# Optimization experiments

Hardware: AMD Instinct MI355X
Metric: run time of the kernel (lower is better)

The kernel has to match this reference:

```python
import jax, jax.numpy as jnp
import numpy as np

I = 2048   # input_size
H = 2048   # hidden_size
O = 1024   # output_size (decode steps AND out-linear width)
LEAK = 0.01  # nn.LeakyReLU default negative_slope


def setup_inputs() -> dict:
    key = jax.random.key(0)
    ks = jax.random.split(key, 13)
    w = lambda k, shape: (jax.random.normal(k, shape, dtype=jnp.float32) * 0.02)
    return {
        "a": jax.random.normal(ks[0], (I,), dtype=jnp.float32),
        # encoder GRU (torch nn.GRU, num_layers=1): gates stacked [r; z; n]
        "enc_Wih": w(ks[1], (3 * H, I)),
        "enc_Whh": w(ks[2], (3 * H, H)),
        "enc_bih": w(ks[3], (3 * H,)),
        "enc_bhh": w(ks[4], (3 * H,)),
        # decoder into: Linear(1 -> H)
        "into_W": w(ks[5], (H, 1)),
        "into_b": w(ks[6], (H,)),
        # decoder GRU
        "dec_Wih": w(ks[7], (3 * H, H)),
        "dec_Whh": w(ks[8], (3 * H, H)),
        "dec_bih": w(ks[9], (3 * H,)),
        "dec_bhh": w(ks[10], (3 * H,)),
        # decoder out: Linear(H -> O)
        "out_W": w(ks[11], (O, H)),
        "out_b": w(ks[12], (O,)),
    }


def _gru_cell(x, h, Wih, Whh, bih, bhh):
    # torch GRU cell: gates ordered [reset; update; new]
    n_h = h.shape[0]
    gx = Wih @ x + bih          # (3H,)
    gh = Whh @ h + bhh          # (3H,)
    r = jax.nn.sigmoid(gx[:n_h] + gh[:n_h])
    z = jax.nn.sigmoid(gx[n_h:2 * n_h] + gh[n_h:2 * n_h])
    n = jnp.tanh(gx[2 * n_h:] + r * gh[2 * n_h:])
    return (1.0 - z) * n + z * h


def reference(a, enc_Wih, enc_Whh, enc_bih, enc_bhh,
              into_W, into_b, dec_Wih, dec_Whh, dec_bih, dec_bhh,
              out_W, out_b):
    n_h = enc_Whh.shape[1]
    n_out = out_W.shape[0]
    # encoder: seq_len=1, batch=1, h0=0 -> single GRU step on the flat input
    h = _gru_cell(a, jnp.zeros((n_h,), a.dtype), enc_Wih, enc_Whh, enc_bih, enc_bhh)

    def step(carry, _):
        h, x = carry                         # h: (H,), x: scalar fed-back topv
        v = into_W[:, 0] * x + into_b        # Linear(1->H) on scalar input
        v = jnp.where(v > 0, v, LEAK * v)    # LeakyReLU
        h = _gru_cell(v, h, dec_Wih, dec_Whh, dec_bih, dec_bhh)
        logits = out_W @ h + out_b           # (O,)
        topv = jnp.max(jax.nn.log_softmax(logits))  # topk(1) value
        return (h, topv), topv

    # torch.empty is uninitialized; use 0.0 as the initial decoder input
    (_, _), outs = jax.lax.scan(step, (h, jnp.zeros((), a.dtype)), None, length=n_out)
    return outs  # (output_size,) sequence of top log-prob values
```

## Files before the change

### kernel.cpp

```cpp
#include <hip/hip_runtime.h>

#define Hs 2048
#define Os 1024
#define NB 256
#define NT 512
#define BSTR 32

typedef unsigned int       uint32;
typedef unsigned long long uint64;
typedef unsigned short     ushort_t;
typedef _Float16 half2v __attribute__((ext_vector_type(2)));

__device__ __forceinline__ ushort_t f2h(float f) {
    _Float16 h = (_Float16)f;
    return __builtin_bit_cast(ushort_t, h);
}

__device__ __forceinline__ uint32 pkh2(float lo, float hi) {
#if __has_builtin(__builtin_amdgcn_cvt_pkrtz)
    return __builtin_bit_cast(uint32, __builtin_amdgcn_cvt_pkrtz(lo, hi));
#else
    return (uint32)f2h(lo) | ((uint32)f2h(hi) << 16);
#endif
}

__device__ __forceinline__ float dot2(uint32 wp, uint32 vp, float acc) {
#if __has_builtin(__builtin_amdgcn_fdot2)
    return __builtin_amdgcn_fdot2(__builtin_bit_cast(half2v, wp),
                                  __builtin_bit_cast(half2v, vp), acc, false);
#else
    half2v a = __builtin_bit_cast(half2v, wp), b = __builtin_bit_cast(half2v, vp);
    acc = fmaf((float)a.x, (float)b.x, acc);
    return fmaf((float)a.y, (float)b.y, acc);
#endif
}

__device__ __forceinline__ float dot8(uint4 wq, uint4 vq, float acc) {
    acc = dot2(wq.x, vq.x, acc); acc = dot2(wq.y, vq.y, acc);
    acc = dot2(wq.z, vq.z, acc); acc = dot2(wq.w, vq.w, acc);
    return acc;
}

__device__ __forceinline__ float dot4f(float4 w, float4 v, float acc) {
    acc = fmaf(w.x, v.x, acc); acc = fmaf(w.y, v.y, acc);
    acc = fmaf(w.z, v.z, acc); acc = fmaf(w.w, v.w, acc);
    return acc;
}

__device__ __forceinline__ int sj(int j) { return j ^ (((j >> 5) & 1) << 2); }

#define KEEP4(u) asm volatile("" : "+v"((u).x), "+v"((u).y), "+v"((u).z), "+v"((u).w))

__device__ __forceinline__ uint32 gload(const uint32* p) {
    return __hip_atomic_load(p, __ATOMIC_RELAXED, __HIP_MEMORY_SCOPE_AGENT);
}
__device__ __forceinline__ void gstore(uint32* p, uint32 v) {
    __hip_atomic_store(p, v, __ATOMIC_RELAXED, __HIP_MEMORY_SCOPE_AGENT);
}
__device__ __forceinline__ uint64 gload64(const uint64* p) {
    return __hip_atomic_load(p, __ATOMIC_RELAXED, __HIP_MEMORY_SCOPE_AGENT);
}
__device__ __forceinline__ void gstore64(uint64* p, uint64 v) {
    __hip_atomic_store(p, v, __ATOMIC_RELAXED, __HIP_MEMORY_SCOPE_AGENT);
}
__device__ __forceinline__ uint64 pack_fe(float f, uint32 ep) {
    return (uint64)__float_as_uint(f) | ((uint64)ep << 32);
}
__device__ __forceinline__ float  pk_val(uint64 v) { return __uint_as_float((uint32)v); }
__device__ __forceinline__ uint32 pk_ep(uint64 v)  { return (uint32)(v >> 32); }

__device__ __forceinline__ uint64 spin_load(const uint64* p, uint32 target) {
    uint64 v = gload64(p);
    while (pk_ep(v) < target) { __builtin_amdgcn_s_sleep(0); v = gload64(p); }
    return v;
}

__device__ __forceinline__ void gridbar(uint32* bs, uint32 epoch, int b) {
    asm volatile("s_waitcnt vmcnt(0)" ::: "memory");
    __syncthreads();
    const int tid = threadIdx.x;
    if (b == 0) {
        if (tid < 64) {
            if (tid == 0) gstore(bs, epoch);
            uint32 a0 = gload(bs + (tid      ) * BSTR);
            uint32 a1 = gload(bs + (tid +  64) * BSTR);
            uint32 a2 = gload(bs + (tid + 128) * BSTR);
            uint32 a3 = gload(bs + (tid + 192) * BSTR);
            while (a0 < epoch) { __builtin_amdgcn_s_sleep(0); a0 = gload(bs + (tid      ) * BSTR); }
            while (a1 < epoch) { __builtin_amdgcn_s_sleep(0); a1 = gload(bs + (tid +  64) * BSTR); }
            while (a2 < epoch) { __builtin_amdgcn_s_sleep(0); a2 = gload(bs + (tid + 128) * BSTR); }
            while (a3 < epoch) { __builtin_amdgcn_s_sleep(0); a3 = gload(bs + (tid + 192) * BSTR); }
            if (tid < 8) gstore(bs + (NB + tid) * BSTR, epoch);
        }
        __syncthreads();
    } else {
        if (tid == 0) {
            gstore(bs + b * BSTR, epoch);
            const uint32* go = bs + (NB + (b & 7)) * BSTR;
            while (gload(go) < epoch) __builtin_amdgcn_s_sleep(0);
        }
        __syncthreads();
    }
    asm volatile("" ::: "memory");
}

__global__ void cvt_kernel(const float* __restrict__ src, ushort_t* __restrict__ dst, int n4) {
    int stride = gridDim.x * blockDim.x;
    for (int idx = blockIdx.x * blockDim.x + threadIdx.x; idx < n4; idx += stride) {
        float4 f = ((const float4*)src)[idx];
        ushort4 o;
        o.x = f2h(f.x); o.y = f2h(f.y); o.z = f2h(f.z); o.w = f2h(f.w);
        ((ushort4*)dst)[idx] = o;
    }
}

__global__ void __launch_bounds__(NT) decode_kernel(
    const float* __restrict__ a,
    const float* __restrict__ encWih,
    const float* __restrict__ encBih,
    const float* __restrict__ encBhh,
    const float* __restrict__ intoW,
    const float* __restrict__ intoB,
    const float* __restrict__ decBih,
    const float* __restrict__ decBhh,
    const float* __restrict__ outB,
    const ushort_t* __restrict__ Wih,
    const ushort_t* __restrict__ Whh,
    const ushort_t* __restrict__ Wout,
    float* __restrict__ hbuf,
    uint64* __restrict__ pm,
    uint64* __restrict__ ps,
    uint32* __restrict__ bstate,
    float* __restrict__ out)
{
    const int tid  = threadIdx.x;
    const int b    = blockIdx.x;
    const int lane = tid & 63;
    const int w    = tid >> 6;
    const int i    = b * 8 + w;

    uint32* hbu = (uint32*)hbuf;

    __shared__ __align__(16) float  h_enc[Hs];
    __shared__ __align__(16) uint32 h16[Hs / 2];
    __shared__ __align__(16) uint32 v16[Hs / 2];
    __shared__ float red_a[8];
    __shared__ float h_own[8];
    __shared__ float xshare;

    uint32 nbar = 0;

    const float bxr = decBih[i], bxz = decBih[i + Hs], bxn = decBih[i + 2 * Hs];
    const float bhr = decBhh[i], bhz = decBhh[i + Hs], bhn = decBhh[i + 2 * Hs];
    const float4 iw4 = ((const float4*)intoW)[tid];
    const float4 ib4 = ((const float4*)intoB)[tid];
    const float ob0 = outB[b * 4 + 0], ob1 = outB[b * 4 + 1], ob2 = outB[b * 4 + 2], ob3 = outB[b * 4 + 3];

    const ushort_t* Xr = Wih + (size_t)i * Hs;
    const ushort_t* Xz = Wih + (size_t)(i + Hs) * Hs;
    const ushort_t* Xn = Wih + (size_t)(i + 2 * Hs) * Hs;
    const ushort_t* Hr = Whh + (size_t)i * Hs;
    const ushort_t* Hz = Whh + (size_t)(i + Hs) * Hs;
    const ushort_t* Hn = Whh + (size_t)(i + 2 * Hs) * Hs;

    for (int k = tid; k < Hs; k += NT) h_enc[sj(k)] = a[k];
    __syncthreads();
    {
        float sr = 0.f, sz = 0.f, sn = 0.f;
        const float* Rr = encWih + (size_t)i * Hs;
        const float* Rz = encWih + (size_t)(i + Hs) * Hs;
        const float* Rn = encWih + (size_t)(i + 2 * Hs) * Hs;
#pragma unroll
        for (int it = 0; it < 4; ++it) {
            int j0 = it * 512 + lane * 8;
            float4 a0 = *(const float4*)(h_enc + sj(j0));
            float4 a1 = *(const float4*)(h_enc + sj(j0 + 4));
            sr = dot4f(*(const float4*)(Rr + j0), a0, sr);
            sr = dot4f(*(const float4*)(Rr + j0 + 4), a1, sr);
            sz = dot4f(*(const float4*)(Rz + j0), a0, sz);
            sz = dot4f(*(const float4*)(Rz + j0 + 4), a1, sz);
            sn = dot4f(*(const float4*)(Rn + j0), a0, sn);
            sn = dot4f(*(const float4*)(Rn + j0 + 4), a1, sn);
        }
#pragma unroll
        for (int m = 1; m < 64; m <<= 1) {
            sr += __shfl_xor(sr, m, 64);
            sz += __shfl_xor(sz, m, 64);
            sn += __shfl_xor(sn, m, 64);
        }
        float gxr = sr + encBih[i];
        float gxz = sz + encBih[i + Hs];
        float gxn = sn + encBih[i + 2 * Hs];
        float r = 1.f / (1.f + __expf(-(gxr + encBhh[i])));
        float z = 1.f / (1.f + __expf(-(gxz + encBhh[i + Hs])));
        float n = tanhf(gxn + r * encBhh[i + 2 * Hs]);
        if (lane == 0) gstore(hbu + i, __float_as_uint((1.f - z) * n));
    }

    uint4 wXr[4], wXz[4], wXn[4], wHr[4], wHz[4], wHn[4], wO[2];
    {
        const ushort_t* R = Wout + (size_t)(b * 4 + (w >> 1)) * Hs + (w & 1) * 1024;
#pragma unroll
        for (int it = 0; it < 4; ++it) {
            int j0 = it * 512 + lane * 8;
            wXr[it] = *(const uint4*)(Xr + j0);
            wXz[it] = *(const uint4*)(Xz + j0);
            wXn[it] = *(const uint4*)(Xn + j0);
            wHr[it] = *(const uint4*)(Hr + j0);
            wHz[it] = *(const uint4*)(Hz + j0);
            wHn[it] = *(const uint4*)(Hn + j0);
        }
#pragma unroll
        for (int it = 0; it < 2; ++it)
            wO[it] = *(const uint4*)(R + it * 512 + lane * 8);
    }

    gridbar(bstate, ++nbar, b);

    {
        uint64 p0 = gload64((const uint64*)hbu + tid);
        uint64 p1 = gload64((const uint64*)hbu + tid + 512);
        if (lane == 0) h_own[w] = __uint_as_float(gload(hbu + i));
        h16[tid]       = pkh2(__uint_as_float((uint32)p0), __uint_as_float((uint32)(p0 >> 32)));
        h16[tid + 512] = pkh2(__uint_as_float((uint32)p1), __uint_as_float((uint32)(p1 >> 32)));
    }
    __syncthreads();

    for (int t = 0; t < Os; ++t) {
        KEEP4(wXr[0]); KEEP4(wXr[1]); KEEP4(wXr[2]); KEEP4(wXr[3]);
        KEEP4(wXz[0]); KEEP4(wXz[1]); KEEP4(wXz[2]); KEEP4(wXz[3]);
        KEEP4(wXn[0]); KEEP4(wXn[1]); KEEP4(wXn[2]); KEEP4(wXn[3]);
        KEEP4(wHr[0]); KEEP4(wHr[1]); KEEP4(wHr[2]); KEEP4(wHr[3]);
        KEEP4(wHz[0]); KEEP4(wHz[1]); KEEP4(wHz[2]); KEEP4(wHz[3]);
        KEEP4(wHn[0]); KEEP4(wHn[1]); KEEP4(wHn[2]); KEEP4(wHn[3]);
        KEEP4(wO[0]);  KEEP4(wO[1]);

        float ahr = 0.f, ahz = 0.f, ahn = 0.f;
#pragma unroll
        for (int it = 0; it < 4; ++it) {
            const uint4 hq = *(const uint4*)(h16 + it * 256 + lane * 4);
            ahr = dot8(wHr[it], hq, ahr);
            ahz = dot8(wHz[it], hq, ahz);
            ahn = dot8(wHn[it], hq, ahn);
        }
#pragma unroll
        for (int m = 1; m < 64; m <<= 1) {
            ahr += __shfl_xor(ahr, m, 64);
            ahz += __shfl_xor(ahz, m, 64);
            ahn += __shfl_xor(ahn, m, 64);
        }
        const float hold = h_own[w];

        if (w == 0) {
            if (t > 0) {
                const uint32 tg = (uint32)t;
                const uint64 *q0 = pm + lane,       *q1 = pm + lane + 64,
                             *q2 = pm + lane + 128, *q3 = pm + lane + 192;
                const uint64 *r0 = ps + lane,       *r1 = ps + lane + 64,
                             *r2 = ps + lane + 128, *r3 = ps + lane + 192;
                uint64 vm0 = gload64(q0), vm1 = gload64(q1), vm2 = gload64(q2), vm3 = gload64(q3);
                uint64 vs0 = gload64(r0), vs1 = gload64(r1), vs2 = gload64(r2), vs3 = gload64(r3);
                while (pk_ep(vm0) < tg) { __builtin_amdgcn_s_sleep(0); vm0 = gload64(q0); }
                while (pk_ep(vm1) < tg) { __builtin_amdgcn_s_sleep(0); vm1 = gload64(q1); }
                while (pk_ep(vm2) < tg) { __builtin_amdgcn_s_sleep(0); vm2 = gload64(q2); }
                while (pk_ep(vm3) < tg) { __builtin_amdgcn_s_sleep(0); vm3 = gload64(q3); }
                while (pk_ep(vs0) < tg) { __builtin_amdgcn_s_sleep(0); vs0 = gload64(r0); }
                while (pk_ep(vs1) < tg) { __builtin_amdgcn_s_sleep(0); vs1 = gload64(r1); }
                while (pk_ep(vs2) < tg) { __builtin_amdgcn_s_sleep(0); vs2 = gload64(r2); }
                while (pk_ep(vs3) < tg) { __builtin_amdgcn_s_sleep(0); vs3 = gload64(r3); }
                float xm = pk_val(vm0), xs = pk_val(vs0);
                {
                    float mo = pk_val(vm1), so = pk_val(vs1);
                    float M = fmaxf(xm, mo);
                    xs = xs * __expf(xm - M) + so * __expf(mo - M); xm = M;
                }
                {
                    float mo = pk_val(vm2), so = pk_val(vs2);
                    float M = fmaxf(xm, mo);
                    xs = xs * __expf(xm - M) + so * __expf(mo - M); xm = M;
                }
                {
                    float mo = pk_val(vm3), so = pk_val(vs3);
                    float M = fmaxf(xm, mo);
                    xs = xs * __expf(xm - M) + so * __expf(mo - M); xm = M;
                }
#pragma unroll
                for (int k = 1; k < 64; k <<= 1) {
                    float mo = __shfl_xor(xm, k, 64);
                    float so = __shfl_xor(xs, k, 64);
                    float M = fmaxf(xm, mo);
                    xs = xs * __expf(xm - M) + so * __expf(mo - M);
                    xm = M;
                }
                if (lane == 0) {
                    float xv = -__logf(xs);
                    xshare = xv;
                    if (b == 0) out[t - 1] = xv;
                }
            } else if (lane == 0) {
                xshare = 0.f;
            }
        }
        __syncthreads();
        const float x = xshare;

        {
            float v0 = fmaf(iw4.x, x, ib4.x); v0 = (v0 > 0.f) ? v0 : 0.01f * v0;
            float v1 = fmaf(iw4.y, x, ib4.y); v1 = (v1 > 0.f) ? v1 : 0.01f * v1;
            float v2 = fmaf(iw4.z, x, ib4.z); v2 = (v2 > 0.f) ? v2 : 0.01f * v2;
            float v3 = fmaf(iw4.w, x, ib4.w); v3 = (v3 > 0.f) ? v3 : 0.01f * v3;
            v16[2 * tid]     = pkh2(v0, v1);
            v16[2 * tid + 1] = pkh2(v2, v3);
        }
        __syncthreads();

        {
            float axr = 0.f, axz = 0.f, axn = 0.f;
#pragma unroll
            for (int it = 0; it < 4; ++it) {
                const uint4 vq = *(const uint4*)(v16 + it * 256 + lane * 4);
                axr = dot8(wXr[it], vq, axr);
                axz = dot8(wXz[it], vq, axz);
                axn = dot8(wXn[it], vq, axn);
            }
#pragma unroll
            for (int m = 1; m < 64; m <<= 1) {
                axr += __shfl_xor(axr, m, 64);
                axz += __shfl_xor(axz, m, 64);
                axn += __shfl_xor(axn, m, 64);
            }
            float r = 1.f / (1.f + __expf(-(axr + bxr + ahr + bhr)));
            float z = 1.f / (1.f + __expf(-(axz + bxz + ahz + bhz)));
            float n = tanhf(axn + bxn + r * (ahn + bhn));
            float hn = (1.f - z) * n + z * hold;
            if (lane == 0) gstore(hbu + i, __float_as_uint(hn));
        }

        gridbar(bstate, ++nbar, b);

        {
            uint64 p0 = gload64((const uint64*)hbu + tid);
            uint64 p1 = gload64((const uint64*)hbu + tid + 512);
            if (lane == 0) h_own[w] = __uint_as_float(gload(hbu + i));
            h16[tid]       = pkh2(__uint_as_float((uint32)p0), __uint_as_float((uint32)(p0 >> 32)));
            h16[tid + 512] = pkh2(__uint_as_float((uint32)p1), __uint_as_float((uint32)(p1 >> 32)));
        }
        __syncthreads();

        {
            const int jbp = (w & 1) * 512;
            float acc = 0.f;
#pragma unroll
            for (int it = 0; it < 2; ++it) {
                const uint4 hq = *(const uint4*)(h16 + jbp + it * 256 + lane * 4);
                acc = dot8(wO[it], hq, acc);
            }
#pragma unroll
            for (int m = 1; m < 64; m <<= 1) acc += __shfl_xor(acc, m, 64);
            if (lane == 0) red_a[w] = acc;
            __syncthreads();
            if (tid == 0) {
                float l0 = red_a[0] + red_a[1] + ob0;
                float l1 = red_a[2] + red_a[3] + ob1;
                float l2 = red_a[4] + red_a[5] + ob2;
                float l3 = red_a[6] + red_a[7] + ob3;
                float m = fmaxf(fmaxf(l0, l1), fmaxf(l2, l3));
                float s = __expf(l0 - m) + __expf(l1 - m) + __expf(l2 - m) + __expf(l3 - m);
                gstore64(pm + b, pack_fe(m, (uint32)(t + 1)));
                gstore64(ps + b, pack_fe(s, (uint32)(t + 1)));
            }
        }
    }

    if (b == 0 && w == 0) {
        float xm = -1e30f, xs = 0.f;
#pragma unroll
        for (int q = 0; q < 4; ++q) {
            int p = lane + q * 64;
            uint64 vm = spin_load(pm + p, (uint32)Os);
            uint64 vs = spin_load(ps + p, (uint32)Os);
            float mo = pk_val(vm), so = pk_val(vs);
            float M = fmaxf(xm, mo);
            xs = xs * __expf(xm - M) + so * __expf(mo - M);
            xm = M;
        }
#pragma unroll
        for (int k = 1; k < 64; k <<= 1) {
            float mo = __shfl_xor(xm, k, 64);
            float so = __shfl_xor(xs, k, 64);
            float M = fmaxf(xm, mo);
            xs = xs * __expf(xm - M) + so * __expf(mo - M);
            xm = M;
        }
        if (lane == 0) out[Os - 1] = -__logf(xs);
    }
}

extern "C" void kernel_launch(void* const* d_in, const int* in_sizes, int n_in,
                              void* d_out, int out_size, void* d_ws, size_t ws_size,
                              hipStream_t stream) {
    const float* a      = (const float*)d_in[0];
    const float* encWih = (const float*)d_in[1];
    const float* encBih = (const float*)d_in[3];
    const float* encBhh = (const float*)d_in[4];
    const float* intoW  = (const float*)d_in[5];
    const float* intoB  = (const float*)d_in[6];
    const float* decWih = (const float*)d_in[7];
    const float* decWhh = (const float*)d_in[8];
    const float* decBih = (const float*)d_in[9];
    const float* decBhh = (const float*)d_in[10];
    const float* outW   = (const float*)d_in[11];
    const float* outB   = (const float*)d_in[12];

    ushort_t* wsWih  = (ushort_t*)d_ws;
    ushort_t* wsWhh  = wsWih + (size_t)3 * Hs * Hs;
    ushort_t* wsWout = wsWhh + (size_t)3 * Hs * Hs;
    float*    hbuf   = (float*)(wsWout + (size_t)Os * Hs);
    uint64*   pmw    = (uint64*)(hbuf + 2 * Hs);
    uint64*   psw    = pmw + NB;
    uint32*   bstate = (uint32*)(psw + NB);
    float*    out    = (float*)d_out;

    cvt_kernel<<<4096, 256, 0, stream>>>(decWih, wsWih, 3 * Hs * Hs / 4);
    cvt_kernel<<<4096, 256, 0, stream>>>(decWhh, wsWhh, 3 * Hs * Hs / 4);
    cvt_kernel<<<1024, 256, 0, stream>>>(outW,  wsWout, Os * Hs / 4);
    hipMemsetAsync(pmw, 0, 2 * NB * sizeof(uint64), stream);
    hipMemsetAsync(bstate, 0, (NB + 8) * BSTR * sizeof(uint32), stream);

    void* args[] = {
        (void*)&a, (void*)&encWih, (void*)&encBih, (void*)&encBhh,
        (void*)&intoW, (void*)&intoB, (void*)&decBih, (void*)&decBhh,
        (void*)&outB, (void*)&wsWih, (void*)&wsWhh, (void*)&wsWout,
        (void*)&hbuf, (void*)&pmw, (void*)&psw, (void*)&bstate, (void*)&out
    };
    hipLaunchCooperativeKernel(reinterpret_cast<void*>(decode_kernel),
                               dim3(NB), dim3(NT), args, 0, stream);
}
```

Measured before the change: 5.626 ms.

## Fuse hidden-state publish with grid barrier via epoch-tagged packed fp16 slots

Replaces the separate per-block arrival flags plus float hidden buffer with epoch-tagged 64-bit slots holding fp16-packed hidden pairs. Block 0 polls all data slots directly, so data arrival doubles as the barrier signal. Each block keeps its own hidden value in registers instead of rereading it. This removes one round of global stores and loads per step and the conversion to fp16 on the consumer side. The cost is that block 0 now polls 1024 slots per step instead of 256 flags, and the shared hidden state is rounded to fp16 with round-toward-zero.

```diff
diff --git a/kernel.cpp b/kernel.cpp
--- a/kernel.cpp
+++ b/kernel.cpp
@@ -73,35 +73,6 @@
     uint64 v = gload64(p);
     while (pk_ep(v) < target) { __builtin_amdgcn_s_sleep(0); v = gload64(p); }
     return v;
-}
-
-__device__ __forceinline__ void gridbar(uint32* bs, uint32 epoch, int b) {
-    asm volatile("s_waitcnt vmcnt(0)" ::: "memory");
-    __syncthreads();
-    const int tid = threadIdx.x;
-    if (b == 0) {
-        if (tid < 64) {
-            if (tid == 0) gstore(bs, epoch);
-            uint32 a0 = gload(bs + (tid      ) * BSTR);
-            uint32 a1 = gload(bs + (tid +  64) * BSTR);
-            uint32 a2 = gload(bs + (tid + 128) * BSTR);
-            uint32 a3 = gload(bs + (tid + 192) * BSTR);
-            while (a0 < epoch) { __builtin_amdgcn_s_sleep(0); a0 = gload(bs + (tid      ) * BSTR); }
-            while (a1 < epoch) { __builtin_amdgcn_s_sleep(0); a1 = gload(bs + (tid +  64) * BSTR); }
-            while (a2 < epoch) { __builtin_amdgcn_s_sleep(0); a2 = gload(bs + (tid + 128) * BSTR); }
-            while (a3 < epoch) { __builtin_amdgcn_s_sleep(0); a3 = gload(bs + (tid + 192) * BSTR); }
-            if (tid < 8) gstore(bs + (NB + tid) * BSTR, epoch);
-        }
-        __syncthreads();
-    } else {
-        if (tid == 0) {
-            gstore(bs + b * BSTR, epoch);
-            const uint32* go = bs + (NB + (b & 7)) * BSTR;
-            while (gload(go) < epoch) __builtin_amdgcn_s_sleep(0);
-        }
-        __syncthreads();
-    }
-    asm volatile("" ::: "memory");
 }
 
 __global__ void cvt_kernel(const float* __restrict__ src, ushort_t* __restrict__ dst, int n4) {
@@ -127,10 +98,10 @@
     const ushort_t* __restrict__ Wih,
     const ushort_t* __restrict__ Whh,
     const ushort_t* __restrict__ Wout,
-    float* __restrict__ hbuf,
+    uint64* __restrict__ hpk,
     uint64* __restrict__ pm,
     uint64* __restrict__ ps,
-    uint32* __restrict__ bstate,
+    uint32* __restrict__ go,
     float* __restrict__ out)
 {
     const int tid  = threadIdx.x;
@@ -139,16 +110,12 @@
     const int w    = tid >> 6;
     const int i    = b * 8 + w;
 
-    uint32* hbu = (uint32*)hbuf;
-
     __shared__ __align__(16) float  h_enc[Hs];
     __shared__ __align__(16) uint32 h16[Hs / 2];
     __shared__ __align__(16) uint32 v16[Hs / 2];
     __shared__ float red_a[8];
-    __shared__ float h_own[8];
+    __shared__ float h_sh[8];
     __shared__ float xshare;
-
-    uint32 nbar = 0;
 
     const float bxr = decBih[i], bxz = decBih[i + Hs], bxn = decBih[i + 2 * Hs];
     const float bhr = decBhh[i], bhz = decBhh[i + Hs], bhn = decBhh[i + 2 * Hs];
@@ -162,6 +129,8 @@
     const ushort_t* Hr = Whh + (size_t)i * Hs;
     const ushort_t* Hz = Whh + (size_t)(i + Hs) * Hs;
     const ushort_t* Hn = Whh + (size_t)(i + 2 * Hs) * Hs;
+
+    float hold;
 
     for (int k = tid; k < Hs; k += NT) h_enc[sj(k)] = a[k];
     __syncthreads();
@@ -194,7 +163,8 @@
         float r = 1.f / (1.f + __expf(-(gxr + encBhh[i])));
         float z = 1.f / (1.f + __expf(-(gxz + encBhh[i + Hs])));
         float n = tanhf(gxn + r * encBhh[i + 2 * Hs]);
-        if (lane == 0) gstore(hbu + i, __float_as_uint((1.f - z) * n));
+        hold = (1.f - z) * n;
+        if (lane == 0) h_sh[w] = hold;
     }
 
     uint4 wXr[4], wXz[4], wXn[4], wHr[4], wHz[4], wHn[4], wO[2];
@@ -215,18 +185,43 @@
             wO[it] = *(const uint4*)(R + it * 512 + lane * 8);
     }
 
-    gridbar(bstate, ++nbar, b);
+    __syncthreads();
+    if (tid < 4) {
+        uint32 pr = pkh2(h_sh[2 * tid], h_sh[2 * tid + 1]);
+        gstore64(hpk + b * 4 + tid, (uint64)pr | (1ull << 32));
+    }
 
     {
-        uint64 p0 = gload64((const uint64*)hbu + tid);
-        uint64 p1 = gload64((const uint64*)hbu + tid + 512);
-        if (lane == 0) h_own[w] = __uint_as_float(gload(hbu + i));
-        h16[tid]       = pkh2(__uint_as_float((uint32)p0), __uint_as_float((uint32)(p0 >> 32)));
-        h16[tid + 512] = pkh2(__uint_as_float((uint32)p1), __uint_as_float((uint32)(p1 >> 32)));
+        if (b == 0) {
+            if (tid < 64) {
+                uint64 va[16];
+#pragma unroll
+                for (int k = 0; k < 16; ++k) va[k] = gload64(hpk + tid + k * 64);
+#pragma unroll
+                for (int k = 0; k < 16; ++k)
+                    while (pk_ep(va[k]) < 1u) { __builtin_amdgcn_s_sleep(0); va[k] = gload64(hpk + tid + k * 64); }
+                if (tid < 8) gstore(go + tid * BSTR, 1u);
+            }
+            __syncthreads();
+        } else {
+            if (tid == 0) {
+                const uint32* g = go + (b & 7) * BSTR;
+                while (gload(g) < 1u) __builtin_amdgcn_s_sleep(0);
+            }
+            __syncthreads();
+        }
+    }
+    {
+        uint64 p0 = gload64(hpk + tid);
+        uint64 p1 = gload64(hpk + tid + 512);
+        h16[tid]       = (uint32)p0;
+        h16[tid + 512] = (uint32)p1;
     }
     __syncthreads();
 
     for (int t = 0; t < Os; ++t) {
+        const uint32 eph = (uint32)t + 2u;
+
         KEEP4(wXr[0]); KEEP4(wXr[1]); KEEP4(wXr[2]); KEEP4(wXr[3]);
         KEEP4(wXz[0]); KEEP4(wXz[1]); KEEP4(wXz[2]); KEEP4(wXz[3]);
         KEEP4(wXn[0]); KEEP4(wXn[1]); KEEP4(wXn[2]); KEEP4(wXn[3]);
@@ -249,7 +244,6 @@
             ahz += __shfl_xor(ahz, m, 64);
             ahn += __shfl_xor(ahn, m, 64);
         }
-        const float hold = h_own[w];
 
         if (w == 0) {
             if (t > 0) {
@@ -333,17 +327,40 @@
             float z = 1.f / (1.f + __expf(-(axz + bxz + ahz + bhz)));
             float n = tanhf(axn + bxn + r * (ahn + bhn));
             float hn = (1.f - z) * n + z * hold;
-            if (lane == 0) gstore(hbu + i, __float_as_uint(hn));
-        }
-
-        gridbar(bstate, ++nbar, b);
+            hold = hn;
+            if (lane == 0) h_sh[w] = hn;
+        }
+        __syncthreads();
+
+        if (tid < 4) {
+            uint32 pr = pkh2(h_sh[2 * tid], h_sh[2 * tid + 1]);
+            gstore64(hpk + b * 4 + tid, (uint64)pr | ((uint64)eph << 32));
+        }
+
+        if (b == 0) {
+            if (tid < 64) {
+                uint64 va[16];
+#pragma unroll
+                for (int k = 0; k < 16; ++k) va[k] = gload64(hpk + tid + k * 64);
+#pragma unroll
+                for (int k = 0; k < 16; ++k)
+                    while (pk_ep(va[k]) < eph) { __builtin_amdgcn_s_sleep(0); va[k] = gload64(hpk + tid + k * 64); }
+                if (tid < 8) gstore(go + tid * BSTR, eph);
+            }
+            __syncthreads();
+        } else {
+            if (tid == 0) {
+                const uint32* g = go + (b & 7) * BSTR;
+                while (gload(g) < eph) __builtin_amdgcn_s_sleep(0);
+            }
+            __syncthreads();
+        }
 
         {
-            uint64 p0 = gload64((const uint64*)hbu + tid);
-            uint64 p1 = gload64((const uint64*)hbu + tid + 512);
-            if (lane == 0) h_own[w] = __uint_as_float(gload(hbu + i));
-            h16[tid]       = pkh2(__uint_as_float((uint32)p0), __uint_as_float((uint32)(p0 >> 32)));
-            h16[tid + 512] = pkh2(__uint_as_float((uint32)p1), __uint_as_float((uint32)(p1 >> 32)));
+            uint64 p0 = gload64(hpk + tid);
+            uint64 p1 = gload64(hpk + tid + 512);
+            h16[tid]       = (uint32)p0;
+            h16[tid + 512] = (uint32)p1;
         }
         __syncthreads();
 
@@ -415,23 +432,22 @@
     ushort_t* wsWih  = (ushort_t*)d_ws;
     ushort_t* wsWhh  = wsWih + (size_t)3 * Hs * Hs;
     ushort_t* wsWout = wsWhh + (size_t)3 * Hs * Hs;
-    float*    hbuf   = (float*)(wsWout + (size_t)Os * Hs);
-    uint64*   pmw    = (uint64*)(hbuf + 2 * Hs);
+    uint64*   hpk    = (uint64*)(wsWout + (size_t)Os * Hs);
+    uint64*   pmw    = hpk + Hs / 2;
     uint64*   psw    = pmw + NB;
-    uint32*   bstate = (uint32*)(psw + NB);
+    uint32*   gow    = (uint32*)(psw + NB);
     float*    out    = (float*)d_out;
 
     cvt_kernel<<<4096, 256, 0, stream>>>(decWih, wsWih, 3 * Hs * Hs / 4);
     cvt_kernel<<<4096, 256, 0, stream>>>(decWhh, wsWhh, 3 * Hs * Hs / 4);
     cvt_kernel<<<1024, 256, 0, stream>>>(outW,  wsWout, Os * Hs / 4);
-    hipMemsetAsync(pmw, 0, 2 * NB * sizeof(uint64), stream);
-    hipMemsetAsync(bstate, 0, (NB + 8) * BSTR * sizeof(uint32), stream);
+    hipMemsetAsync(hpk, 0, (Hs / 2 + 2 * NB) * sizeof(uint64) + 8 * BSTR * sizeof(uint32), stream);
 
     void* args[] = {
         (void*)&a, (void*)&encWih, (void*)&encBih, (void*)&encBhh,
         (void*)&intoW, (void*)&intoB, (void*)&decBih, (void*)&decBhh,
         (void*)&outB, (void*)&wsWih, (void*)&wsWhh, (void*)&wsWout,
-        (void*)&hbuf, (void*)&pmw, (void*)&psw, (void*)&bstate, (void*)&out
+        (void*)&hpk, (void*)&pmw, (void*)&psw, (void*)&gow, (void*)&out
     };
     hipLaunchCooperativeKernel(reinterpret_cast<void*>(decode_kernel),
                                dim3(NB), dim3(NT), args, 0, stream);
```

After: 5.433 ms. -3.4%, faster.
